# Kernel tuning notes

Hardware: AMD Instinct MI355X
Metric: run time of the kernel (lower is better)

Reference implementation:

```python
import jax, jax.numpy as jnp
import numpy as np

N = 50000      # nodes
E = 400000     # edges
D = 256        # args.dimensions
H1 = 32        # hidden1 (per-head)
HEADS = 4      # gat_heads
H2 = 64        # hidden2
DEC = 512      # decoder1
B = 4096       # number of entity index pairs
NEG = 0.2      # PyG GATConv leaky_relu negative slope


def setup_inputs() -> dict:
    key = jax.random.key(0)
    ks = jax.random.split(key, 24)
    s = lambda k, shape, fan: jax.random.normal(k, shape, jnp.float32) * (1.0 / np.sqrt(fan))
    return {
        "x_o": jax.random.normal(ks[0], (N, D), jnp.float32),
        "x_a": jax.random.normal(ks[1], (N, D), jnp.float32),
        "edge_index": jax.random.randint(ks[2], (2, E), 0, N, jnp.int32),
        "idx": jax.random.randint(ks[3], (2, B), 0, N, jnp.int32),
        # GATConv 1: in D -> H1 per head, HEADS heads, concat
        "W1": s(ks[4], (D, HEADS * H1), D),
        "a_src1": s(ks[5], (HEADS, H1), H1),
        "a_dst1": s(ks[6], (HEADS, H1), H1),
        "b1": jnp.zeros((HEADS * H1,), jnp.float32),
        "p1": jnp.full((HEADS * H1,), 0.25, jnp.float32),   # PReLU weight
        # GATConv 2: HEADS*H1 -> H2, 1 head, no concat
        "W2": s(ks[7], (HEADS * H1, H2), HEADS * H1),
        "a_src2": s(ks[8], (1, H2), H2),
        "a_dst2": s(ks[9], (1, H2), H2),
        "b2": jnp.zeros((H2,), jnp.float32),
        "p2": jnp.full((H2,), 0.25, jnp.float32),
        # mlp1
        "mlp_W": s(ks[10], (H2, H2), H2),
        "mlp_b": jnp.zeros((H2,), jnp.float32),
        # Discriminator bilinear (out=1)
        "disc_W": s(ks[11], (H2, H2), H2),
        "disc_b": jnp.zeros((), jnp.float32),
        # adversarial_logits linear (fixed, deterministic stand-in)
        "adv_W": s(ks[12], (H2, H2), H2),
        "adv_b": jnp.zeros((H2,), jnp.float32),
        # fusion decoder (stand-in for build_fusion_decoder): MLP with 2 heads
        "f_W1": s(ks[13], (2 * H2, DEC), 2 * H2),
        "f_b1": jnp.zeros((DEC,), jnp.float32),
        "f_W2": s(ks[14], (DEC, 2), DEC),
        "f_b2": jnp.zeros((2,), jnp.float32),
        "f_W3": s(ks[15], (DEC, 2), DEC),
        "f_b3": jnp.zeros((2,), jnp.float32),
    }


def prelu(x, w):
    return jnp.where(x >= 0, x, w * x)


def gat_conv(x, src, dst, W, a_src, a_dst, b, heads, out_dim, concat):
    # PyG GATConv (eval): per-head linear, edge attention, dst-segment softmax, scatter-sum.
    n = x.shape[0]
    h = (x @ W).reshape(n, heads, out_dim)                  # [N, H, F]
    a_s = (h * a_src[None]).sum(-1)                         # [N, H]
    a_d = (h * a_dst[None]).sum(-1)                         # [N, H]
    e = jax.nn.leaky_relu(a_s[src] + a_d[dst], NEG)         # [E', H]
    e_max = jax.ops.segment_max(e, dst, num_segments=n)
    w = jnp.exp(e - e_max[dst])
    denom = jax.ops.segment_sum(w, dst, num_segments=n)
    alpha = w / (denom[dst] + 1e-16)                        # [E', H]
    out = jax.ops.segment_sum(h[src] * alpha[..., None], dst, num_segments=n)  # [N, H, F]
    out = out.reshape(n, heads * out_dim) if concat else out.mean(1)
    return out + b


def encode(x, src, dst, W1, a_src1, a_dst1, b1, p1, W2, a_src2, a_dst2, b2, p2):
    x1 = prelu(gat_conv(x, src, dst, W1, a_src1, a_dst1, b1, HEADS, H1, True), p1)
    x2 = gat_conv(x1, src, dst, W2, a_src2, a_dst2, b2, 1, H2, False)
    return prelu(x2, p2)


def discriminate(c, h_pl, h_mi, disc_W, disc_b):
    # nn.Bilinear(n_h, n_h, 1) against broadcast summary c
    Wc = disc_W @ c                                          # [H2]
    sc_1 = h_pl @ Wc + disc_b                                # [N]
    sc_2 = h_mi @ Wc + disc_b                                # [N]
    return jnp.stack([sc_1, sc_2], axis=1)                   # [N, 2]


def reference(x_o, x_a, edge_index, idx,
              W1, a_src1, a_dst1, b1, p1,
              W2, a_src2, a_dst2, b2, p2,
              mlp_W, mlp_b, disc_W, disc_b, adv_W, adv_b,
              f_W1, f_b1, f_W2, f_b2, f_W3, f_b3):
    n = x_o.shape[0]
    loops = jnp.arange(n, dtype=edge_index.dtype)            # PyG add_self_loops=True
    src = jnp.concatenate([edge_index[0], loops])
    dst = jnp.concatenate([edge_index[1], loops])

    x2_o = encode(x_o, src, dst, W1, a_src1, a_dst1, b1, p1, W2, a_src2, a_dst2, b2, p2)
    x2_o_a = encode(x_a, src, dst, W1, a_src1, a_dst1, b1, p1, W2, a_src2, a_dst2, b2, p2)

    h_os = jax.nn.sigmoid(x2_o.mean(0)) @ mlp_W + mlp_b      # AvgReadout -> sigmoid -> mlp1
    h_os_a = jax.nn.sigmoid(x2_o_a.mean(0)) @ mlp_W + mlp_b

    ret_os = discriminate(h_os, x2_o, x2_o_a, disc_W, disc_b)
    ret_os_a = discriminate(h_os_a, x2_o_a, x2_o, disc_W, disc_b)

    # entities (task_type 'other' branch)
    e1 = x2_o[idx[0]]
    e2 = x2_o[idx[1]]
    fh = jax.nn.relu(jnp.concatenate([e1, e2], axis=-1) @ f_W1 + f_b1)
    log = fh @ f_W2 + f_b2
    log1 = fh @ f_W3 + f_b3

    sc_1 = (x2_o @ adv_W + adv_b).sum(1)[None, :]            # [1, N]
    sc_2 = (x2_o_a @ adv_W + adv_b).sum(1)[None, :]
    logits = jnp.concatenate([sc_1, sc_2], axis=1)           # [1, 2N]

    return (log, ret_os, ret_os_a, x2_o, logits, log1)
```

## Files before the change

kernel.cpp:

```cpp
#include <hip/hip_runtime.h>
#include <hip/hip_bf16.h>
#include <math.h>

constexpr int NN   = 50000;
constexpr int N2   = 2*NN;
constexpr int EE   = 400000;
constexpr int DIN  = 256;
constexpr int M1   = 128;
constexpr int H1N  = 4;
constexpr int M2   = 64;
constexpr int BP   = 4096;
constexpr int DEC  = 512;
constexpr float SLOPE = 0.2f;

constexpr int O_LOG    = 0;
constexpr int O_RETOS  = 8192;
constexpr int O_RETOSA = 108192;
constexpr int O_X2     = 208192;
constexpr int O_LOGITS = 3408192;
constexpr int O_LOG1   = 3508192;

constexpr int SCAN_NB = (NN + 1023) / 1024;

typedef __attribute__((ext_vector_type(8))) short short8;
typedef __attribute__((ext_vector_type(4))) float f32x4;

__device__ __forceinline__ short f2bs(float v){
    __hip_bfloat16 h = __float2bfloat16(v);
    unsigned short u; __builtin_memcpy(&u, &h, 2);
    return (short)u;
}
__device__ __forceinline__ float lrelu(float e){ return (e >= 0.f) ? e : SLOPE*e; }

__global__ void hist_dst(const int* __restrict__ edst, int* __restrict__ cnt){
    int i = blockIdx.x*blockDim.x + threadIdx.x;
    if (i < EE) atomicAdd(&cnt[edst[i]], 1);
}

__global__ __launch_bounds__(1024) void scan_blk(const int* __restrict__ cnt,
                                                 int* __restrict__ rowex,
                                                 int* __restrict__ bsum){
    __shared__ int wsum[16];
    const int t = threadIdx.x;
    const int idx = blockIdx.x*1024 + t;
    const int lane = t & 63, wid = t >> 6;
    int v = (idx < NN) ? cnt[idx] : 0;
    int s = v;
    #pragma unroll
    for (int o = 1; o < 64; o <<= 1){
        int u = __shfl_up(s, o, 64);
        if (lane >= o) s += u;
    }
    if (lane == 63) wsum[wid] = s;
    __syncthreads();
    if (wid == 0){
        int ws = (lane < 16) ? wsum[lane] : 0;
        #pragma unroll
        for (int o = 1; o < 16; o <<= 1){
            int u = __shfl_up(ws, o, 64);
            if (lane >= o) ws += u;
        }
        if (lane < 16) wsum[lane] = ws;
    }
    __syncthreads();
    int base = (wid > 0) ? wsum[wid-1] : 0;
    int incl = base + s;
    if (idx < NN) rowex[idx] = incl - v;
    if (t == 1023) bsum[blockIdx.x] = incl;
}

__global__ void scan_bsum(int* __restrict__ bsum, int nb){
    const int lane = threadIdx.x;
    int v = (lane < nb) ? bsum[lane] : 0;
    int s = v;
    #pragma unroll
    for (int o = 1; o < 64; o <<= 1){
        int u = __shfl_up(s, o, 64);
        if (lane >= o) s += u;
    }
    if (lane < nb) bsum[lane] = s - v;
}

__global__ void scan_fix(int* __restrict__ row, const int* __restrict__ bsum,
                         int* __restrict__ cursor){
    int idx = blockIdx.x*blockDim.x + threadIdx.x;
    if (idx < NN){
        int r = row[idx] + bsum[idx >> 10];
        row[idx] = r;
        cursor[idx] = r;
    }
    if (idx == 0) row[NN] = EE;
}

__global__ void fill_csr(const int* __restrict__ esrc, const int* __restrict__ edst,
                         int* __restrict__ cursor, int* __restrict__ adj){
    int i = blockIdx.x*blockDim.x + threadIdx.x;
    if (i >= EE) return;
    int d = edst[i];
    int slot = atomicAdd(&cursor[d], 1);
    adj[slot] = esrc[i];
}

__device__ __forceinline__ void pack_one(const float* __restrict__ W,
                                         __hip_bfloat16* __restrict__ Wpk,
                                         int i, int M){
    int k = i / M, c = i - k*M;
    int kb = k >> 5, r = k & 31, quad = r >> 3, j = r & 7;
    int ct = c >> 4, ln = quad*16 + (c & 15);
    int CT = M >> 4;
    size_t dst = (((size_t)kb*CT + ct)*64 + ln)*8 + j;
    Wpk[dst] = __float2bfloat16(W[i]);
}

__global__ void pack_all(const float* __restrict__ W1, const float* __restrict__ W2,
                         const float* __restrict__ fW1,
                         __hip_bfloat16* __restrict__ Wpk1,
                         __hip_bfloat16* __restrict__ Wpk2,
                         __hip_bfloat16* __restrict__ Wpkf){
    constexpr int S1 = DIN*M1;
    constexpr int S2 = S1 + M1*M2;
    constexpr int S3 = S2 + M1*DEC;
    int i = blockIdx.x*blockDim.x + threadIdx.x;
    if (i < S1)       pack_one(W1,  Wpk1, i,      M1);
    else if (i < S2)  pack_one(W2,  Wpk2, i - S1, M2);
    else if (i < S3)  pack_one(fW1, Wpkf, i - S2, DEC);
}

template<int K, int M, int HEADS_T, bool AF32>
__global__ __launch_bounds__(256) void gemm_attn(
        const void* __restrict__ X0, const void* __restrict__ X1,
        const __hip_bfloat16* __restrict__ Wpk,
        const float* __restrict__ asrc, const float* __restrict__ adst,
        __hip_bfloat16* __restrict__ Hb,
        float* __restrict__ AS, float* __restrict__ AD){
    constexpr int CT = M/16;
    constexpr int KB = K/32;
    constexpr int CPH = CT/HEADS_T;
    const int wave = (blockIdx.x*256 + threadIdx.x) >> 6;
    const int lane = threadIdx.x & 63;
    const int n0 = wave*16;
    if (n0 >= N2) return;
    const int arow = lane & 15;
    const int quad = lane >> 4;

    f32x4 acc[CT];
    #pragma unroll
    for (int ct = 0; ct < CT; ++ct) acc[ct] = (f32x4){0.f,0.f,0.f,0.f};

    const float* apf = nullptr;
    const __hip_bfloat16* apb = nullptr;
    if constexpr (AF32){
        apf = (n0 < NN) ? ((const float*)X0 + (size_t)(n0 + arow)*K)
                        : ((const float*)X1 + (size_t)(n0 - NN + arow)*K);
    } else {
        apb = (const __hip_bfloat16*)X0 + (size_t)(n0 + arow)*K;
    }

    for (int kb = 0; kb < KB; ++kb){
        const int kbase = kb*32 + quad*8;
        short8 af;
        if constexpr (AF32){
            float4 v0 = *(const float4*)(apf + kbase);
            float4 v1 = *(const float4*)(apf + kbase + 4);
            af[0]=f2bs(v0.x); af[1]=f2bs(v0.y); af[2]=f2bs(v0.z); af[3]=f2bs(v0.w);
            af[4]=f2bs(v1.x); af[5]=f2bs(v1.y); af[6]=f2bs(v1.z); af[7]=f2bs(v1.w);
        } else {
            af = *(const short8*)(apb + kbase);
        }
        const __hip_bfloat16* wp = Wpk + (size_t)kb*CT*64*8;
        #pragma unroll
        for (int ct = 0; ct < CT; ++ct){
            short8 bfr = *(const short8*)(wp + ((size_t)ct*64 + lane)*8);
            acc[ct] = __builtin_amdgcn_mfma_f32_16x16x32_bf16(af, bfr, acc[ct], 0, 0, 0);
        }
    }

    #pragma unroll
    for (int ct = 0; ct < CT; ++ct){
        #pragma unroll
        for (int r = 0; r < 4; ++r){
            int n = n0 + quad*4 + r;
            Hb[(size_t)n*M + ct*16 + arow] = __float2bfloat16(acc[ct][r]);
        }
    }

    float a_s[CT], a_d[CT];
    #pragma unroll
    for (int ct = 0; ct < CT; ++ct){
        a_s[ct] = asrc[ct*16 + arow];
        a_d[ct] = adst[ct*16 + arow];
    }
    #pragma unroll
    for (int r = 0; r < 4; ++r){
        const int n = n0 + quad*4 + r;
        #pragma unroll
        for (int h = 0; h < HEADS_T; ++h){
            float ss = 0.f, dd = 0.f;
            #pragma unroll
            for (int c2 = 0; c2 < CPH; ++c2){
                int ct = h*CPH + c2;
                ss += acc[ct][r]*a_s[ct];
                dd += acc[ct][r]*a_d[ct];
            }
            #pragma unroll
            for (int o = 8; o > 0; o >>= 1){
                ss += __shfl_down(ss, o, 16);
                dd += __shfl_down(dd, o, 16);
            }
            if (arow == 0){
                AS[(size_t)n*HEADS_T + h] = ss;
                AD[(size_t)n*HEADS_T + h] = dd;
            }
        }
    }
}

__global__ __launch_bounds__(256) void gat_agg_l1(
        const int* __restrict__ row, const int* __restrict__ adj,
        const __hip_bfloat16* __restrict__ Hfeat,
        const float* __restrict__ AS, const float* __restrict__ AD,
        const float* __restrict__ b, const float* __restrict__ p,
        __hip_bfloat16* __restrict__ outB){
    const int wv = (blockIdx.x*blockDim.x + threadIdx.x) >> 6;
    const int nw = (gridDim.x*blockDim.x) >> 6;
    const int t = threadIdx.x & 63;
    const int h = t >> 4;
    const unsigned* Hw = (const unsigned*)Hfeat;
    const float bb0 = b[2*t], bb1 = b[2*t+1];
    const float pp0 = p[2*t], pp1 = p[2*t+1];
    for (int nd = wv; nd < N2; nd += nw){
        const int g  = (nd < NN) ? nd : nd - NN;
        const int fb = nd - g;
        const float ad_h = AD[(size_t)nd*4 + h];
        float acc0, acc1, den;
        {
            float ws = __expf(lrelu(AS[(size_t)nd*4 + h] + ad_h));
            unsigned u = Hw[(size_t)nd*64 + t];
            acc0 = __uint_as_float(u << 16) * ws;
            acc1 = __uint_as_float(u & 0xffff0000u) * ws;
            den = ws;
        }
        const int beg = row[g], end = row[g+1];
        int j = beg;
        for (; j + 3 < end; j += 4){
            int s0 = adj[j]   + fb;
            int s1 = adj[j+1] + fb;
            int s2 = adj[j+2] + fb;
            int s3 = adj[j+3] + fb;
            float e0 = AS[(size_t)s0*4 + h];
            float e1 = AS[(size_t)s1*4 + h];
            float e2 = AS[(size_t)s2*4 + h];
            float e3 = AS[(size_t)s3*4 + h];
            unsigned u0 = Hw[(size_t)s0*64 + t];
            unsigned u1 = Hw[(size_t)s1*64 + t];
            unsigned u2 = Hw[(size_t)s2*64 + t];
            unsigned u3 = Hw[(size_t)s3*64 + t];
            float w0 = __expf(lrelu(e0 + ad_h));
            float w1 = __expf(lrelu(e1 + ad_h));
            float w2 = __expf(lrelu(e2 + ad_h));
            float w3 = __expf(lrelu(e3 + ad_h));
            acc0 += __uint_as_float(u0 << 16) * w0;
            acc1 += __uint_as_float(u0 & 0xffff0000u) * w0;
            acc0 += __uint_as_float(u1 << 16) * w1;
            acc1 += __uint_as_float(u1 & 0xffff0000u) * w1;
            acc0 += __uint_as_float(u2 << 16) * w2;
            acc1 += __uint_as_float(u2 & 0xffff0000u) * w2;
            acc0 += __uint_as_float(u3 << 16) * w3;
            acc1 += __uint_as_float(u3 & 0xffff0000u) * w3;
            den += w0 + w1 + w2 + w3;
        }
        for (; j < end; ++j){
            int s = adj[j] + fb;
            float wgt = __expf(lrelu(AS[(size_t)s*4 + h] + ad_h));
            unsigned u = Hw[(size_t)s*64 + t];
            acc0 += __uint_as_float(u << 16) * wgt;
            acc1 += __uint_as_float(u & 0xffff0000u) * wgt;
            den += wgt;
        }
        float inv = 1.f/(den + 1e-16f);
        float v0 = acc0*inv + bb0;
        float v1 = acc1*inv + bb1;
        v0 = (v0 >= 0.f) ? v0 : pp0*v0;
        v1 = (v1 >= 0.f) ? v1 : pp1*v1;
        ushort2 st = make_ushort2((unsigned short)f2bs(v0), (unsigned short)f2bs(v1));
        *(ushort2*)(outB + (size_t)nd*128 + 2*t) = st;
    }
}

__global__ __launch_bounds__(256) void gat_agg_l2(
        const int* __restrict__ row, const int* __restrict__ adj,
        const __hip_bfloat16* __restrict__ Hfeat,
        const float* __restrict__ AS, const float* __restrict__ AD,
        const float* __restrict__ b, const float* __restrict__ p,
        float* __restrict__ outO, float* __restrict__ outA){
    const int wv = (blockIdx.x*blockDim.x + threadIdx.x) >> 6;
    const int nw = (gridDim.x*blockDim.x) >> 6;
    const int t = threadIdx.x & 63;
    const float bb = b[t], pp = p[t];
    const ushort* Hu = (const ushort*)Hfeat;
    for (int nd = wv; nd < N2; nd += nw){
        const int g  = (nd < NN) ? nd : nd - NN;
        const int fb = nd - g;
        const float ad_d = AD[nd];
        float acc, den;
        {
            float ws = __expf(lrelu(AS[nd] + ad_d));
            unsigned u = Hu[(size_t)nd*64 + t];
            acc = __uint_as_float(u << 16) * ws;
            den = ws;
        }
        const int beg = row[g], end = row[g+1];
        int j = beg;
        for (; j + 3 < end; j += 4){
            int s0 = adj[j]   + fb;
            int s1 = adj[j+1] + fb;
            int s2 = adj[j+2] + fb;
            int s3 = adj[j+3] + fb;
            float e0 = AS[s0];
            float e1 = AS[s1];
            float e2 = AS[s2];
            float e3 = AS[s3];
            unsigned u0 = Hu[(size_t)s0*64 + t];
            unsigned u1 = Hu[(size_t)s1*64 + t];
            unsigned u2 = Hu[(size_t)s2*64 + t];
            unsigned u3 = Hu[(size_t)s3*64 + t];
            float w0 = __expf(lrelu(e0 + ad_d));
            float w1 = __expf(lrelu(e1 + ad_d));
            float w2 = __expf(lrelu(e2 + ad_d));
            float w3 = __expf(lrelu(e3 + ad_d));
            acc += __uint_as_float(u0 << 16) * w0;
            acc += __uint_as_float(u1 << 16) * w1;
            acc += __uint_as_float(u2 << 16) * w2;
            acc += __uint_as_float(u3 << 16) * w3;
            den += w0 + w1 + w2 + w3;
        }
        for (; j < end; ++j){
            int s = adj[j] + fb;
            float wgt = __expf(lrelu(AS[s] + ad_d));
            unsigned u = Hu[(size_t)s*64 + t];
            acc += __uint_as_float(u << 16) * wgt;
            den += wgt;
        }
        float v = acc/(den + 1e-16f) + bb;
        v = (v >= 0.f) ? v : pp*v;
        if (nd < NN) outO[(size_t)nd*64 + t] = v;
        else         outA[(size_t)(nd - NN)*64 + t] = v;
    }
}

__global__ __launch_bounds__(256) void colsum2(const float* __restrict__ Xo,
                                               const float* __restrict__ Xa,
                                               float* __restrict__ outO,
                                               float* __restrict__ outA){
    __shared__ float red[2][256];
    const int t = threadIdx.x;
    const int c = t & 63;
    const int rg = t >> 6;
    float so = 0.f, sa = 0.f;
    for (int r = blockIdx.x*4 + rg; r < NN; r += gridDim.x*4){
        so += Xo[(size_t)r*64 + c];
        sa += Xa[(size_t)r*64 + c];
    }
    red[0][t] = so; red[1][t] = sa; __syncthreads();
    if (t < 64){
        atomicAdd(&outO[c], red[0][t] + red[0][t+64] + red[0][t+128] + red[0][t+192]);
        atomicAdd(&outA[c], red[1][t] + red[1][t+64] + red[1][t+128] + red[1][t+192]);
    }
}

__global__ void summary(const float* __restrict__ csum_o, const float* __restrict__ csum_a,
                        const float* __restrict__ mlpW, const float* __restrict__ mlpb,
                        const float* __restrict__ discW,
                        const float* __restrict__ advW, const float* __restrict__ advb,
                        float* __restrict__ Wc_o, float* __restrict__ Wc_a,
                        float* __restrict__ advRow, float* __restrict__ advbsum){
    __shared__ float s_o[64], s_a[64], h_o[64], h_a[64];
    const int t = threadIdx.x;
    s_o[t] = 1.f/(1.f + expf(-csum_o[t]/(float)NN));
    s_a[t] = 1.f/(1.f + expf(-csum_a[t]/(float)NN));
    __syncthreads();
    float ao = 0.f, aa = 0.f;
    for (int k = 0; k < 64; ++k){ float w = mlpW[k*64 + t]; ao += s_o[k]*w; aa += s_a[k]*w; }
    float bb = mlpb[t];
    h_o[t] = ao + bb; h_a[t] = aa + bb;
    __syncthreads();
    float wo = 0.f, wa = 0.f;
    for (int j = 0; j < 64; ++j){ float w = discW[t*64 + j]; wo += w*h_o[j]; wa += w*h_a[j]; }
    Wc_o[t] = wo; Wc_a[t] = wa;
    float ar = 0.f;
    for (int j = 0; j < 64; ++j) ar += advW[t*64 + j];
    advRow[t] = ar;
    float ab = advb[t];
    for (int o = 32; o > 0; o >>= 1) ab += __shfl_down(ab, o, 64);
    if (t == 0) advbsum[0] = ab;
}

__global__ void node_outputs(const float* __restrict__ x2o, const float* __restrict__ x2a,
                             const float* __restrict__ Wc_o, const float* __restrict__ Wc_a,
                             const float* __restrict__ advRow, const float* __restrict__ advbsum,
                             const float* __restrict__ discb,
                             float* __restrict__ out){
    const int n = blockIdx.x*4 + (threadIdx.x >> 6);
    const int l = threadIdx.x & 63;
    float xo = x2o[(size_t)n*64 + l], xa = x2a[(size_t)n*64 + l];
    float wo = Wc_o[l], wa = Wc_a[l], ar = advRow[l];
    float d1 = xo*wo, d2 = xa*wo, d3 = xa*wa, d4 = xo*wa, d5 = xo*ar, d6 = xa*ar;
    for (int o = 32; o > 0; o >>= 1){
        d1 += __shfl_down(d1, o, 64); d2 += __shfl_down(d2, o, 64);
        d3 += __shfl_down(d3, o, 64); d4 += __shfl_down(d4, o, 64);
        d5 += __shfl_down(d5, o, 64); d6 += __shfl_down(d6, o, 64);
    }
    if (l == 0){
        float db = discb[0];
        float ab = advbsum[0];
        out[O_RETOS  + n*2 + 0] = d1 + db;
        out[O_RETOS  + n*2 + 1] = d2 + db;
        out[O_RETOSA + n*2 + 0] = d3 + db;
        out[O_RETOSA + n*2 + 1] = d4 + db;
        out[O_LOGITS + n]       = d5 + ab;
        out[O_LOGITS + NN + n]  = d6 + ab;
    }
}

__global__ __launch_bounds__(256) void decoder_fused(
        const float* __restrict__ x2o, const int* __restrict__ idxArr,
        const __hip_bfloat16* __restrict__ Wpkf, const float* __restrict__ fb1,
        const float* __restrict__ fW2, const float* __restrict__ fb2,
        const float* __restrict__ fW3, const float* __restrict__ fb3,
        float* __restrict__ out){
    __shared__ float part[4][16][4];
    const int t = threadIdx.x;
    const int wid = t >> 6, lane = t & 63;
    const int arow = lane & 15, quad = lane >> 4;
    const int p0 = blockIdx.x*16;
    const int i0 = idxArr[p0 + arow];
    const int i1 = idxArr[BP + p0 + arow];

    f32x4 acc[8];
    #pragma unroll
    for (int c = 0; c < 8; ++c) acc[c] = (f32x4){0.f,0.f,0.f,0.f};

    #pragma unroll
    for (int kb = 0; kb < 4; ++kb){
        int src = (kb < 2) ? i0 : i1;
        int koff = (kb & 1)*32 + quad*8;
        const float* ap = x2o + (size_t)src*64 + koff;
        float4 v0 = *(const float4*)ap;
        float4 v1 = *(const float4*)(ap + 4);
        short8 af;
        af[0]=f2bs(v0.x); af[1]=f2bs(v0.y); af[2]=f2bs(v0.z); af[3]=f2bs(v0.w);
        af[4]=f2bs(v1.x); af[5]=f2bs(v1.y); af[6]=f2bs(v1.z); af[7]=f2bs(v1.w);
        const __hip_bfloat16* wp = Wpkf + (size_t)kb*32*64*8;
        #pragma unroll
        for (int c = 0; c < 8; ++c){
            int ct = wid*8 + c;
            short8 bfr = *(const short8*)(wp + ((size_t)ct*64 + lane)*8);
            acc[c] = __builtin_amdgcn_mfma_f32_16x16x32_bf16(af, bfr, acc[c], 0, 0, 0);
        }
    }

    float a0[4] = {0,0,0,0}, a1[4] = {0,0,0,0};
    float c0[4] = {0,0,0,0}, c1[4] = {0,0,0,0};
    #pragma unroll
    for (int c = 0; c < 8; ++c){
        int col = wid*128 + c*16 + arow;
        float bb = fb1[col];
        float w20 = fW2[col*2], w21 = fW2[col*2+1];
        float w30 = fW3[col*2], w31 = fW3[col*2+1];
        #pragma unroll
        for (int r = 0; r < 4; ++r){
            float v = acc[c][r] + bb;
            v = (v > 0.f) ? v : 0.f;
            a0[r] += v*w20; a1[r] += v*w21;
            c0[r] += v*w30; c1[r] += v*w31;
        }
    }
    #pragma unroll
    for (int o = 8; o > 0; o >>= 1){
        #pragma unroll
        for (int r = 0; r < 4; ++r){
            a0[r] += __shfl_down(a0[r], o, 16);
            a1[r] += __shfl_down(a1[r], o, 16);
            c0[r] += __shfl_down(c0[r], o, 16);
            c1[r] += __shfl_down(c1[r], o, 16);
        }
    }
    if (arow == 0){
        #pragma unroll
        for (int r = 0; r < 4; ++r){
            part[wid][quad*4 + r][0] = a0[r];
            part[wid][quad*4 + r][1] = a1[r];
            part[wid][quad*4 + r][2] = c0[r];
            part[wid][quad*4 + r][3] = c1[r];
        }
    }
    __syncthreads();
    if (t < 64){
        int pr = t >> 2, o = t & 3;
        float s = part[0][pr][o] + part[1][pr][o] + part[2][pr][o] + part[3][pr][o];
        int gb = p0 + pr;
        if (o == 0)      out[O_LOG  + gb*2 + 0] = s + fb2[0];
        else if (o == 1) out[O_LOG  + gb*2 + 1] = s + fb2[1];
        else if (o == 2) out[O_LOG1 + gb*2 + 0] = s + fb3[0];
        else             out[O_LOG1 + gb*2 + 1] = s + fb3[1];
    }
}

extern "C" void kernel_launch(void* const* d_in, const int* in_sizes, int n_in,
                              void* d_out, int out_size, void* d_ws, size_t ws_size,
                              hipStream_t stream){
    const float* x_o    = (const float*)d_in[0];
    const float* x_a    = (const float*)d_in[1];
    const int*   edge   = (const int*)d_in[2];
    const int*   idxp   = (const int*)d_in[3];
    const float* W1     = (const float*)d_in[4];
    const float* a_src1 = (const float*)d_in[5];
    const float* a_dst1 = (const float*)d_in[6];
    const float* b1     = (const float*)d_in[7];
    const float* p1     = (const float*)d_in[8];
    const float* W2     = (const float*)d_in[9];
    const float* a_src2 = (const float*)d_in[10];
    const float* a_dst2 = (const float*)d_in[11];
    const float* b2     = (const float*)d_in[12];
    const float* p2     = (const float*)d_in[13];
    const float* mlpW   = (const float*)d_in[14];
    const float* mlpb   = (const float*)d_in[15];
    const float* discW  = (const float*)d_in[16];
    const float* discb  = (const float*)d_in[17];
    const float* advW   = (const float*)d_in[18];
    const float* advb   = (const float*)d_in[19];
    const float* fW1    = (const float*)d_in[20];
    const float* fb1    = (const float*)d_in[21];
    const float* fW2    = (const float*)d_in[22];
    const float* fb2    = (const float*)d_in[23];
    const float* fW3    = (const float*)d_in[24];
    const float* fb3    = (const float*)d_in[25];

    const int* esrc = edge;
    const int* edst = edge + EE;

    float* w = (float*)d_ws;
    size_t off = 0;
    auto alloc = [&](size_t nfloats){ float* p = w + off; off += nfloats; return p; };
    __hip_bfloat16* Hb   = (__hip_bfloat16*)alloc((size_t)N2*M1/2);
    __hip_bfloat16* x1b  = (__hip_bfloat16*)alloc((size_t)N2*M1/2);
    float* asb   = alloc((size_t)N2*H1N);
    float* adb   = alloc((size_t)N2*H1N);
    __hip_bfloat16* Wpk1 = (__hip_bfloat16*)alloc((size_t)DIN*M1/2);
    __hip_bfloat16* Wpk2 = (__hip_bfloat16*)alloc((size_t)M1*M2/2);
    __hip_bfloat16* Wpkf = (__hip_bfloat16*)alloc((size_t)M1*DEC/2);
    int*   cnt   = (int*)alloc(NN);
    int*   row   = (int*)alloc(NN + 1);
    int*   cursor= (int*)alloc(NN);
    int*   adj   = (int*)alloc(EE);
    int*   bsum  = (int*)alloc(SCAN_NB + 1);
    float* smallb= alloc(512);
    float* csum_o = smallb;       float* csum_a = smallb + 64;
    float* Wc_o   = smallb + 128; float* Wc_a   = smallb + 192;
    float* advRow = smallb + 256; float* advbs  = smallb + 320;

    float* x2a = (float*)x1b;

    float* out = (float*)d_out;
    float* x2o = out + O_X2;

    hipMemsetAsync(cnt, 0, NN*sizeof(int), stream);
    hipMemsetAsync(smallb, 0, 128*sizeof(float), stream);
    hist_dst<<<(EE + 255)/256, 256, 0, stream>>>(edst, cnt);
    scan_blk<<<SCAN_NB, 1024, 0, stream>>>(cnt, row, bsum);
    scan_bsum<<<1, 64, 0, stream>>>(bsum, SCAN_NB);
    scan_fix<<<(NN + 255)/256, 256, 0, stream>>>(row, bsum, cursor);
    fill_csr<<<(EE + 255)/256, 256, 0, stream>>>(esrc, edst, cursor, adj);
    pack_all<<<(DIN*M1 + M1*M2 + M1*DEC + 255)/256, 256, 0, stream>>>(
        W1, W2, fW1, Wpk1, Wpk2, Wpkf);

    const int gw = ((N2/16) + 3) / 4;

    gemm_attn<DIN, M1, H1N, true><<<gw, 256, 0, stream>>>(
        x_o, x_a, Wpk1, a_src1, a_dst1, Hb, asb, adb);
    gat_agg_l1<<<2048, 256, 0, stream>>>(row, adj, Hb, asb, adb, b1, p1, x1b);

    gemm_attn<M1, M2, 1, false><<<gw, 256, 0, stream>>>(
        x1b, nullptr, Wpk2, a_src2, a_dst2, Hb, asb, adb);
    gat_agg_l2<<<2048, 256, 0, stream>>>(row, adj, Hb, asb, adb, b2, p2, x2o, x2a);

    colsum2<<<256, 256, 0, stream>>>(x2o, x2a, csum_o, csum_a);
    summary<<<1, 64, 0, stream>>>(csum_o, csum_a, mlpW, mlpb, discW, advW, advb,
                                  Wc_o, Wc_a, advRow, advbs);
    node_outputs<<<NN/4, 256, 0, stream>>>(x2o, x2a, Wc_o, Wc_a, advRow, advbs, discb, out);
    decoder_fused<<<BP/16, 256, 0, stream>>>(x2o, idxp, Wpkf, fb1, fW2, fb2, fW3, fb3, out);
}
```

Baseline: 417.5 us.

## Process two 16-row tiles per wave in gemm_attn with register prefetch

```diff
diff --git a/kernel.cpp b/kernel.cpp
--- a/kernel.cpp
+++ b/kernel.cpp
@@ -138,49 +138,79 @@
     constexpr int CPH = CT/HEADS_T;
     const int wave = (blockIdx.x*256 + threadIdx.x) >> 6;
     const int lane = threadIdx.x & 63;
-    const int n0 = wave*16;
+    const int n0 = wave*32;
     if (n0 >= N2) return;
     const int arow = lane & 15;
     const int quad = lane >> 4;
 
-    f32x4 acc[CT];
-    #pragma unroll
-    for (int ct = 0; ct < CT; ++ct) acc[ct] = (f32x4){0.f,0.f,0.f,0.f};
-
-    const float* apf = nullptr;
-    const __hip_bfloat16* apb = nullptr;
+    f32x4 acc[2][CT];
+    #pragma unroll
+    for (int t = 0; t < 2; ++t)
+        #pragma unroll
+        for (int ct = 0; ct < CT; ++ct) acc[t][ct] = (f32x4){0.f,0.f,0.f,0.f};
+
+    const float* apf0 = nullptr; const float* apf1 = nullptr;
+    const __hip_bfloat16* apb0 = nullptr; const __hip_bfloat16* apb1 = nullptr;
     if constexpr (AF32){
-        apf = (n0 < NN) ? ((const float*)X0 + (size_t)(n0 + arow)*K)
-                        : ((const float*)X1 + (size_t)(n0 - NN + arow)*K);
+        const int r0 = n0, r1 = n0 + 16;
+        apf0 = ((r0 < NN) ? ((const float*)X0 + (size_t)(r0 + arow)*K)
+                          : ((const float*)X1 + (size_t)(r0 - NN + arow)*K)) + quad*8;
+        apf1 = ((r1 < NN) ? ((const float*)X0 + (size_t)(r1 + arow)*K)
+                          : ((const float*)X1 + (size_t)(r1 - NN + arow)*K)) + quad*8;
     } else {
-        apb = (const __hip_bfloat16*)X0 + (size_t)(n0 + arow)*K;
-    }
-
+        apb0 = (const __hip_bfloat16*)X0 + (size_t)(n0 + arow)*K + quad*8;
+        apb1 = (const __hip_bfloat16*)X0 + (size_t)(n0 + 16 + arow)*K + quad*8;
+    }
+
+    float4 ra00, ra01, ra10, ra11;
+    short8 rb0, rb1;
+    if constexpr (AF32){
+        ra00 = *(const float4*)(apf0);     ra01 = *(const float4*)(apf0 + 4);
+        ra10 = *(const float4*)(apf1);     ra11 = *(const float4*)(apf1 + 4);
+    } else {
+        rb0 = *(const short8*)(apb0);
+        rb1 = *(const short8*)(apb1);
+    }
+
+    #pragma unroll
     for (int kb = 0; kb < KB; ++kb){
-        const int kbase = kb*32 + quad*8;
-        short8 af;
+        short8 af0, af1;
         if constexpr (AF32){
-            float4 v0 = *(const float4*)(apf + kbase);
-            float4 v1 = *(const float4*)(apf + kbase + 4);
-            af[0]=f2bs(v0.x); af[1]=f2bs(v0.y); af[2]=f2bs(v0.z); af[3]=f2bs(v0.w);
-            af[4]=f2bs(v1.x); af[5]=f2bs(v1.y); af[6]=f2bs(v1.z); af[7]=f2bs(v1.w);
+            af0[0]=f2bs(ra00.x); af0[1]=f2bs(ra00.y); af0[2]=f2bs(ra00.z); af0[3]=f2bs(ra00.w);
+            af0[4]=f2bs(ra01.x); af0[5]=f2bs(ra01.y); af0[6]=f2bs(ra01.z); af0[7]=f2bs(ra01.w);
+            af1[0]=f2bs(ra10.x); af1[1]=f2bs(ra10.y); af1[2]=f2bs(ra10.z); af1[3]=f2bs(ra10.w);
+            af1[4]=f2bs(ra11.x); af1[5]=f2bs(ra11.y); af1[6]=f2bs(ra11.z); af1[7]=f2bs(ra11.w);
         } else {
-            af = *(const short8*)(apb + kbase);
+            af0 = rb0; af1 = rb1;
+        }
+        if (kb + 1 < KB){
+            const int kn = (kb + 1)*32;
+            if constexpr (AF32){
+                ra00 = *(const float4*)(apf0 + kn);  ra01 = *(const float4*)(apf0 + kn + 4);
+                ra10 = *(const float4*)(apf1 + kn);  ra11 = *(const float4*)(apf1 + kn + 4);
+            } else {
+                rb0 = *(const short8*)(apb0 + kn);
+                rb1 = *(const short8*)(apb1 + kn);
+            }
         }
         const __hip_bfloat16* wp = Wpk + (size_t)kb*CT*64*8;
         #pragma unroll
         for (int ct = 0; ct < CT; ++ct){
             short8 bfr = *(const short8*)(wp + ((size_t)ct*64 + lane)*8);
-            acc[ct] = __builtin_amdgcn_mfma_f32_16x16x32_bf16(af, bfr, acc[ct], 0, 0, 0);
-        }
-    }
-
-    #pragma unroll
-    for (int ct = 0; ct < CT; ++ct){
-        #pragma unroll
-        for (int r = 0; r < 4; ++r){
-            int n = n0 + quad*4 + r;
-            Hb[(size_t)n*M + ct*16 + arow] = __float2bfloat16(acc[ct][r]);
+            acc[0][ct] = __builtin_amdgcn_mfma_f32_16x16x32_bf16(af0, bfr, acc[0][ct], 0, 0, 0);
+            acc[1][ct] = __builtin_amdgcn_mfma_f32_16x16x32_bf16(af1, bfr, acc[1][ct], 0, 0, 0);
+        }
+    }
+
+    #pragma unroll
+    for (int t = 0; t < 2; ++t){
+        #pragma unroll
+        for (int ct = 0; ct < CT; ++ct){
+            #pragma unroll
+            for (int r = 0; r < 4; ++r){
+                int n = n0 + t*16 + quad*4 + r;
+                Hb[(size_t)n*M + ct*16 + arow] = __float2bfloat16(acc[t][ct][r]);
+            }
         }
     }
 
@@ -191,25 +221,28 @@
         a_d[ct] = adst[ct*16 + arow];
     }
     #pragma unroll
-    for (int r = 0; r < 4; ++r){
-        const int n = n0 + quad*4 + r;
-        #pragma unroll
-        for (int h = 0; h < HEADS_T; ++h){
-            float ss = 0.f, dd = 0.f;
+    for (int t = 0; t < 2; ++t){
+        #pragma unroll
+        for (int r = 0; r < 4; ++r){
+            const int n = n0 + t*16 + quad*4 + r;
             #pragma unroll
-            for (int c2 = 0; c2 < CPH; ++c2){
-                int ct = h*CPH + c2;
-                ss += acc[ct][r]*a_s[ct];
-                dd += acc[ct][r]*a_d[ct];
-            }
-            #pragma unroll
-            for (int o = 8; o > 0; o >>= 1){
-                ss += __shfl_down(ss, o, 16);
-                dd += __shfl_down(dd, o, 16);
-            }
-            if (arow == 0){
-                AS[(size_t)n*HEADS_T + h] = ss;
-                AD[(size_t)n*HEADS_T + h] = dd;
+            for (int h = 0; h < HEADS_T; ++h){
+                float ss = 0.f, dd = 0.f;
+                #pragma unroll
+                for (int c2 = 0; c2 < CPH; ++c2){
+                    int ct = h*CPH + c2;
+                    ss += acc[t][ct][r]*a_s[ct];
+                    dd += acc[t][ct][r]*a_d[ct];
+                }
+                #pragma unroll
+                for (int o = 8; o > 0; o >>= 1){
+                    ss += __shfl_down(ss, o, 16);
+                    dd += __shfl_down(dd, o, 16);
+                }
+                if (arow == 0){
+                    AS[(size_t)n*HEADS_T + h] = ss;
+                    AD[(size_t)n*HEADS_T + h] = dd;
+                }
             }
         }
     }
@@ -574,7 +607,7 @@
     pack_all<<<(DIN*M1 + M1*M2 + M1*DEC + 255)/256, 256, 0, stream>>>(
         W1, W2, fW1, Wpk1, Wpk2, Wpkf);
 
-    const int gw = ((N2/16) + 3) / 4;
+    const int gw = ((N2/32) + 3) / 4;
 
     gemm_attn<DIN, M1, H1N, true><<<gw, 256, 0, stream>>>(
         x_o, x_a, Wpk1, a_src1, a_dst1, Hb, asb, adb);
```

Measured after the change: 417.7 us. No clear change (+0.1%).
